# Kernel optimization log

Hardware: AMD Instinct MI355X
Metric: run time of the kernel (lower is better)

## Reference

```python
import jax, jax.numpy as jnp
import numpy as np

NUM_CLASSES = 80


def setup_inputs() -> dict:
    key = jax.random.key(0)
    k1, k2, k3, k4, k5 = jax.random.split(key, 5)
    B, N, C, H, W = 8, 100, 256, 160, 160
    IMG = 1024
    features = jax.random.normal(k1, (B, C, H, W), dtype=jnp.float32)
    # two random corner points per box -> (x1,y1,x2,y2) with x1<=x2, y1<=y2 (image coords)
    pts = jax.random.uniform(k2, (B, N, 2, 2), minval=0.0, maxval=float(IMG))
    lo = jnp.min(pts, axis=2)  # [B,N,2] -> (x1,y1)
    hi = jnp.max(pts, axis=2)  # [B,N,2] -> (x2,y2)
    boxes = jnp.concatenate([lo, hi], axis=-1).astype(jnp.float32)  # [B,N,4]
    gt_classes = jax.random.randint(k3, (B, N), 0, NUM_CLASSES, dtype=jnp.int32)
    neg_y = jax.random.randint(k4, (B, NUM_CLASSES), 0, H, dtype=jnp.int32)
    neg_x = jax.random.randint(k5, (B, NUM_CLASSES), 0, W, dtype=jnp.int32)
    return {"features": features, "boxes": boxes, "gt_classes": gt_classes,
            "neg_y": neg_y, "neg_x": neg_x, "image_h": IMG, "image_w": IMG}


def reference(features, boxes, gt_classes, neg_y, neg_x, image_h, image_w):
    B, C, H, W = features.shape
    N = boxes.shape[1]
    # scale boxes from image coords to feature-map coords, then truncate like .int()
    scale = jnp.array([W / image_w, H / image_h, W / image_w, H / image_h],
                      dtype=features.dtype)
    sb = boxes * scale
    x1 = jnp.clip(jnp.floor(sb[..., 0]), 0, W).astype(jnp.int32)
    y1 = jnp.clip(jnp.floor(sb[..., 1]), 0, H).astype(jnp.int32)
    x2 = jnp.clip(jnp.floor(sb[..., 2]), 0, W).astype(jnp.int32)
    y2 = jnp.clip(jnp.floor(sb[..., 3]), 0, H).astype(jnp.int32)
    valid = (x2 > x1) & (y2 > y1)  # feature_map.numel() > 0 in the original

    # integral image for O(1) per-box region sums (== adaptive_avg_pool2d to 1x1)
    sat = jnp.cumsum(jnp.cumsum(features, axis=2), axis=3)
    sat = jnp.pad(sat, ((0, 0), (0, 0), (1, 0), (1, 0)))  # [B,C,H+1,W+1]

    def gather_corners(sat_b, y1b, x1b, y2b, x2b):
        # sat_b: [C,H+1,W+1]; returns per-box region sums [C,N]
        return (sat_b[:, y2b, x2b] - sat_b[:, y1b, x2b]
                - sat_b[:, y2b, x1b] + sat_b[:, y1b, x1b])

    box_sum = jax.vmap(gather_corners)(sat, y1, x1, y2, x2)  # [B,C,N]
    area = jnp.maximum((x2 - x1) * (y2 - y1), 1).astype(features.dtype)  # [B,N]
    pooled = (box_sum / area[:, None, :]).transpose(0, 2, 1)  # [B,N,C]
    vmask = valid.astype(features.dtype)
    pooled = pooled * vmask[..., None]

    # scatter-mean into per-(image, class) buckets
    seg = (jnp.arange(B, dtype=jnp.int32)[:, None] * NUM_CLASSES + gt_classes).reshape(-1)
    wsum = jax.ops.segment_sum(pooled.reshape(B * N, C), seg,
                               num_segments=B * NUM_CLASSES)  # [B*80,C]
    cnt = jax.ops.segment_sum(vmask.reshape(-1), seg, num_segments=B * NUM_CLASSES)
    mean = (wsum / jnp.maximum(cnt, 1.0)[:, None]).reshape(B, NUM_CLASSES, C)

    # negative sample (random pixel feature) for empty classes
    neg = jax.vmap(lambda f, ys, xs: f[:, ys, xs].T)(features, neg_y, neg_x)  # [B,80,C]
    out = jnp.where(cnt.reshape(B, NUM_CLASSES, 1) > 0, mean, neg)
    return out
```

## Files before the change

kernel.cpp:

```cpp
#include <hip/hip_runtime.h>

namespace {
constexpr int B  = 8;
constexpr int N  = 100;
constexpr int C  = 256;
constexpr int H  = 160;
constexpr int W  = 160;
constexpr int NC = 80;
constexpr int T  = 1024;
constexpr int NW = 16;
constexpr int RPW = H / NW;
constexpr int SCR = 164;
}

__device__ inline float read_dim(const int* p) {
    int i = *p;
    if (i >= 1 && i <= (1 << 26)) return (float)i;
    return __int_as_float(i);
}

extern "C" __global__ void __launch_bounds__(T)
vpe_kernel(const float* __restrict__ features,
           const float* __restrict__ boxes,
           const int*   __restrict__ gt,
           const int*   __restrict__ neg_y,
           const int*   __restrict__ neg_x,
           const int*   __restrict__ imh_p,
           const int*   __restrict__ imw_p,
           float*       __restrict__ out)
{
    __shared__ float rs[NW * SCR];
    __shared__ float cls_sum[NC];
    __shared__ int   cls_cnt[NC];
    __shared__ int   bx1m[N], bx2m[N], by1[N], by2[N], bcls[N];
    __shared__ float bwgt[N];

    const int tid  = threadIdx.x;
    const int wave = tid >> 6, lane = tid & 63;
    const int b    = blockIdx.x / C;
    const int c    = blockIdx.x % C;
    const float* plane = features + (size_t)(b * C + c) * (H * W);

    if (tid < NC) { cls_sum[tid] = 0.f; cls_cnt[tid] = 0; }
    __syncthreads();

    if (tid < N) {
        float imw = read_dim(imw_p), imh = read_dim(imh_p);
        float sx = (float)W / imw, sy = (float)H / imh;
        const float* bp = boxes + (size_t)(b * N + tid) * 4;
        int x1 = (int)fminf(fmaxf(floorf(bp[0] * sx), 0.f), (float)W);
        int y1 = (int)fminf(fmaxf(floorf(bp[1] * sy), 0.f), (float)H);
        int x2 = (int)fminf(fmaxf(floorf(bp[2] * sx), 0.f), (float)W);
        int y2 = (int)fminf(fmaxf(floorf(bp[3] * sy), 0.f), (float)H);
        bool valid = (x2 > x1) && (y2 > y1);
        bx1m[tid] = x1 - 1; bx2m[tid] = x2 - 1;
        by1[tid] = y1; by2[tid] = y2;
        int cls = gt[b * N + tid];
        bcls[tid] = valid ? cls : -1;
        bwgt[tid] = 1.f / (float)max((x2 - x1) * (y2 - y1), 1);
        if (valid) atomicAdd(&cls_cnt[cls], 1);
    }
    __syncthreads();
    if (tid < N && bcls[tid] >= 0)
        bwgt[tid] /= (float)max(cls_cnt[bcls[tid]], 1);
    __syncthreads();

    float* myrs = &rs[wave * SCR];
    const int nA = lane, nB = lane + 64;
    const int clsA = bcls[nA];
    const int y1A = by1[nA], y2A = by2[nA], x1A = bx1m[nA], x2A = bx2m[nA];
    const float wA = bwgt[nA];
    int clsB = -1, y1B = 0, y2B = 0, x1B = 0, x2B = 0; float wB = 0.f;
    if (nB < N) {
        clsB = bcls[nB]; y1B = by1[nB]; y2B = by2[nB];
        x1B = bx1m[nB]; x2B = bx2m[nB]; wB = bwgt[nB];
    }

    float accA = 0.f, accB = 0.f;
    const bool ldr = (lane < W / 4);

    float4 v = ldr ? ((const float4*)(plane + (size_t)wave * W))[lane]
                   : make_float4(0.f, 0.f, 0.f, 0.f);
    for (int r = 0; r < RPW; ++r) {
        const int y = wave + (r << 4);
        float4 vn = make_float4(0.f, 0.f, 0.f, 0.f);
        if (r + 1 < RPW && ldr)
            vn = ((const float4*)(plane + (size_t)(y + NW) * W))[lane];

        float t = v.x + v.y + v.z + v.w;
        float s = t;
        #pragma unroll
        for (int d = 1; d < 64; d <<= 1) {
            float u = __shfl_up(s, d, 64);
            if (lane >= d) s += u;
        }
        float e  = s - t;
        float p0 = e + v.x, p1 = p0 + v.y, p2 = p1 + v.z, p3 = p2 + v.w;
        if (ldr) *((float4*)(myrs + (lane << 2))) = make_float4(p0, p1, p2, p3);
        __builtin_amdgcn_wave_barrier();

        if (clsA >= 0 && y >= y1A && y < y2A) {
            float hi = myrs[x2A];
            float lo = (x1A >= 0) ? myrs[x1A] : 0.f;
            accA += hi - lo;
        }
        if (clsB >= 0 && y >= y1B && y < y2B) {
            float hi = myrs[x2B];
            float lo = (x1B >= 0) ? myrs[x1B] : 0.f;
            accB += hi - lo;
        }
        __builtin_amdgcn_wave_barrier();
        v = vn;
    }

    if (clsA >= 0) atomicAdd(&cls_sum[clsA], accA * wA);
    if (clsB >= 0) atomicAdd(&cls_sum[clsB], accB * wB);
    __syncthreads();

    if (tid < NC) {
        int cnt = cls_cnt[tid];
        float o = (cnt > 0) ? cls_sum[tid]
                            : plane[neg_y[b * NC + tid] * W + neg_x[b * NC + tid]];
        out[((size_t)b * NC + tid) * C + c] = o;
    }
}

extern "C" void kernel_launch(void* const* d_in, const int* in_sizes, int n_in,
                              void* d_out, int out_size, void* d_ws, size_t ws_size,
                              hipStream_t stream) {
    (void)in_sizes; (void)n_in; (void)d_ws; (void)ws_size; (void)out_size;
    vpe_kernel<<<dim3(B * C), dim3(T), 0, stream>>>(
        (const float*)d_in[0],
        (const float*)d_in[1],
        (const int*)d_in[2],
        (const int*)d_in[3],
        (const int*)d_in[4],
        (const int*)d_in[5],
        (const int*)d_in[6],
        (float*)d_out);
}
```

Measured before the change: 309.3 us.

## Replace per-row scan with 4-row chunk column prefix and per-box column sums

Instead of each wave computing a full row prefix scan for every row and every box testing each row, the kernel now sums 4-row chunks per column into shared memory and prefix-sums them down columns. Each box is then handled by one wave that adds chunk-prefix differences per column, plus raw global reads for at most 3 partial rows at the top and 3 at the bottom. Block size drops to 512 threads with a launch-bounds occupancy hint. The trade is that per-box work now scales with box width and the edge-row reads go back to global memory, and the load is uneven across waves.

```diff
diff --git a/kernel.cpp b/kernel.cpp
--- a/kernel.cpp
+++ b/kernel.cpp
@@ -1,16 +1,16 @@
 #include <hip/hip_runtime.h>
 
 namespace {
-constexpr int B  = 8;
-constexpr int N  = 100;
-constexpr int C  = 256;
-constexpr int H  = 160;
-constexpr int W  = 160;
-constexpr int NC = 80;
-constexpr int T  = 1024;
-constexpr int NW = 16;
-constexpr int RPW = H / NW;
-constexpr int SCR = 164;
+constexpr int B   = 8;
+constexpr int N   = 100;
+constexpr int C   = 256;
+constexpr int H   = 160;
+constexpr int W   = 160;
+constexpr int NC  = 80;
+constexpr int T   = 512;
+constexpr int NWV = 8;
+constexpr int CHR = 4;
+constexpr int NCH = H / CHR;
 }
 
 __device__ inline float read_dim(const int* p) {
@@ -19,7 +19,7 @@
     return __int_as_float(i);
 }
 
-extern "C" __global__ void __launch_bounds__(T)
+extern "C" __global__ void __launch_bounds__(T, 4)
 vpe_kernel(const float* __restrict__ features,
            const float* __restrict__ boxes,
            const int*   __restrict__ gt,
@@ -29,14 +29,14 @@
            const int*   __restrict__ imw_p,
            float*       __restrict__ out)
 {
-    __shared__ float rs[NW * SCR];
+    __shared__ float pre[(NCH + 1) * W];
     __shared__ float cls_sum[NC];
     __shared__ int   cls_cnt[NC];
-    __shared__ int   bx1m[N], bx2m[N], by1[N], by2[N], bcls[N];
+    __shared__ int   bx1[N], bw[N], by1[N], by2[N], bcls[N];
     __shared__ float bwgt[N];
 
     const int tid  = threadIdx.x;
-    const int wave = tid >> 6, lane = tid & 63;
+    const int wv   = tid >> 6, lane = tid & 63;
     const int b    = blockIdx.x / C;
     const int c    = blockIdx.x % C;
     const float* plane = features + (size_t)(b * C + c) * (H * W);
@@ -53,68 +53,71 @@
         int x2 = (int)fminf(fmaxf(floorf(bp[2] * sx), 0.f), (float)W);
         int y2 = (int)fminf(fmaxf(floorf(bp[3] * sy), 0.f), (float)H);
         bool valid = (x2 > x1) && (y2 > y1);
-        bx1m[tid] = x1 - 1; bx2m[tid] = x2 - 1;
-        by1[tid] = y1; by2[tid] = y2;
+        bx1[tid] = x1; bw[tid] = x2 - x1; by1[tid] = y1; by2[tid] = y2;
         int cls = gt[b * N + tid];
         bcls[tid] = valid ? cls : -1;
         bwgt[tid] = 1.f / (float)max((x2 - x1) * (y2 - y1), 1);
         if (valid) atomicAdd(&cls_cnt[cls], 1);
     }
+
+    if (tid < 320) {
+        const int g = tid / 40, xq = tid - g * 40;
+        const float4* p4 = (const float4*)plane;
+        #pragma unroll
+        for (int cc = 0; cc < 5; ++cc) {
+            const int ch = g * 5 + cc;
+            float4 a0 = p4[(ch * CHR + 0) * 40 + xq];
+            float4 a1 = p4[(ch * CHR + 1) * 40 + xq];
+            float4 a2 = p4[(ch * CHR + 2) * 40 + xq];
+            float4 a3 = p4[(ch * CHR + 3) * 40 + xq];
+            float4 s = make_float4(a0.x + a1.x + a2.x + a3.x,
+                                   a0.y + a1.y + a2.y + a3.y,
+                                   a0.z + a1.z + a2.z + a3.z,
+                                   a0.w + a1.w + a2.w + a3.w);
+            *((float4*)&pre[ch * W + xq * 4]) = s;
+        }
+    }
     __syncthreads();
+
     if (tid < N && bcls[tid] >= 0)
         bwgt[tid] /= (float)max(cls_cnt[bcls[tid]], 1);
+
+    if (tid < W) {
+        float run = 0.f;
+        #pragma unroll 8
+        for (int ch = 0; ch < NCH; ++ch) {
+            float v = pre[ch * W + tid];
+            pre[ch * W + tid] = run;
+            run += v;
+        }
+        pre[NCH * W + tid] = run;
+    }
     __syncthreads();
 
-    float* myrs = &rs[wave * SCR];
-    const int nA = lane, nB = lane + 64;
-    const int clsA = bcls[nA];
-    const int y1A = by1[nA], y2A = by2[nA], x1A = bx1m[nA], x2A = bx2m[nA];
-    const float wA = bwgt[nA];
-    int clsB = -1, y1B = 0, y2B = 0, x1B = 0, x2B = 0; float wB = 0.f;
-    if (nB < N) {
-        clsB = bcls[nB]; y1B = by1[nB]; y2B = by2[nB];
-        x1B = bx1m[nB]; x2B = bx2m[nB]; wB = bwgt[nB];
+    for (int n = wv; n < N; n += NWV) {
+        const int cls = bcls[n];
+        if (cls < 0) continue;
+        const int x1 = bx1[n], w = bw[n];
+        const int y1 = by1[n], y2 = by2[n];
+        int chA = (y1 + CHR - 1) / CHR, chB = y2 / CHR;
+        int rt0, rt1, rb0, rb1;
+        bool full = chA < chB;
+        if (full) { rt0 = y1; rt1 = chA * CHR; rb0 = chB * CHR; rb1 = y2; }
+        else      { rt0 = y1; rt1 = y2;        rb0 = 0;         rb1 = 0;  }
+
+        float s = 0.f;
+        for (int xo = lane; xo < w; xo += 64) {
+            const int x = x1 + xo;
+            float t = 0.f;
+            if (full) t += pre[chB * W + x] - pre[chA * W + x];
+            for (int y = rt0; y < rt1; ++y) t += plane[y * W + x];
+            for (int y = rb0; y < rb1; ++y) t += plane[y * W + x];
+            s += t;
+        }
+        #pragma unroll
+        for (int d = 1; d < 64; d <<= 1) s += __shfl_xor(s, d, 64);
+        if (lane == 0) atomicAdd(&cls_sum[cls], s * bwgt[n]);
     }
-
-    float accA = 0.f, accB = 0.f;
-    const bool ldr = (lane < W / 4);
-
-    float4 v = ldr ? ((const float4*)(plane + (size_t)wave * W))[lane]
-                   : make_float4(0.f, 0.f, 0.f, 0.f);
-    for (int r = 0; r < RPW; ++r) {
-        const int y = wave + (r << 4);
-        float4 vn = make_float4(0.f, 0.f, 0.f, 0.f);
-        if (r + 1 < RPW && ldr)
-            vn = ((const float4*)(plane + (size_t)(y + NW) * W))[lane];
-
-        float t = v.x + v.y + v.z + v.w;
-        float s = t;
-        #pragma unroll
-        for (int d = 1; d < 64; d <<= 1) {
-            float u = __shfl_up(s, d, 64);
-            if (lane >= d) s += u;
-        }
-        float e  = s - t;
-        float p0 = e + v.x, p1 = p0 + v.y, p2 = p1 + v.z, p3 = p2 + v.w;
-        if (ldr) *((float4*)(myrs + (lane << 2))) = make_float4(p0, p1, p2, p3);
-        __builtin_amdgcn_wave_barrier();
-
-        if (clsA >= 0 && y >= y1A && y < y2A) {
-            float hi = myrs[x2A];
-            float lo = (x1A >= 0) ? myrs[x1A] : 0.f;
-            accA += hi - lo;
-        }
-        if (clsB >= 0 && y >= y1B && y < y2B) {
-            float hi = myrs[x2B];
-            float lo = (x1B >= 0) ? myrs[x1B] : 0.f;
-            accB += hi - lo;
-        }
-        __builtin_amdgcn_wave_barrier();
-        v = vn;
-    }
-
-    if (clsA >= 0) atomicAdd(&cls_sum[clsA], accA * wA);
-    if (clsB >= 0) atomicAdd(&cls_sum[clsB], accB * wB);
     __syncthreads();
 
     if (tid < NC) {
```

Result: slower. 365.1 us (+18.0%).
